# Optimization experiments

Hardware: AMD Instinct MI355X
Metric: run time of the kernel (lower is better)

Reference implementation:

```python
import jax, jax.numpy as jnp
import numpy as np

EPS = 1e-4  # BatchNorm2d eps from source


def binarize(x):
    # brevitas 1-bit quant: sign(x) with sign(0)=+1; straight-through (clipped) estimator
    y = jnp.clip(x, -1.0, 1.0)
    q = jnp.where(x >= 0, 1.0, -1.0).astype(x.dtype)
    return y + jax.lax.stop_gradient(q - y)


def bn(x, g, b, m, v):
    inv = g / jnp.sqrt(v + EPS)
    return x * inv[None, :, None, None] + (b - m * inv)[None, :, None, None]


def conv(x, w, pad):
    return jax.lax.conv_general_dilated(
        x, w, window_strides=(1, 1), padding=[(pad, pad), (pad, pad)],
        dimension_numbers=('NCHW', 'OIHW', 'NCHW'))


def conv_mod(x, w1, bn1, w3, bn3):
    # conv1x1(binary W) -> BN -> binarize act -> conv3x3(binary W) -> BN -> binarize act
    x = conv(x, binarize(w1), 0)
    x = binarize(bn(x, *bn1))
    x = conv(x, binarize(w3), 1)
    x = binarize(bn(x, *bn3))
    return x


def maxpool2(x):
    return jax.lax.reduce_window(x, -jnp.inf, jax.lax.max,
                                 (1, 1, 2, 2), (1, 1, 2, 2), 'VALID')


def setup_inputs() -> dict:
    key = jax.random.key(0)
    ks = jax.random.split(key, 24)
    B, Cin, down, up, H, W = 16, 256, 64, 256, 56, 56
    d = {
        'x':   jax.random.normal(ks[0], (B, Cin, H, W), jnp.float32),
        'w11': jax.random.normal(ks[1], (down, Cin, 1, 1), jnp.float32) * 0.1,
        'w31': jax.random.normal(ks[2], (up, down, 3, 3), jnp.float32) * 0.1,
        'w12': jax.random.normal(ks[3], (down, up, 1, 1), jnp.float32) * 0.1,
        'w32': jax.random.normal(ks[4], (up, down, 3, 3), jnp.float32) * 0.1,
    }
    # BatchNorm params (inference stats): gamma, beta, running mean, running var
    for i, (tag, c) in enumerate([('11', down), ('31', up), ('12', down), ('32', up)]):
        d['g' + tag] = jax.random.uniform(ks[5 + 4 * i], (c,), jnp.float32, 0.5, 1.5)
        d['b' + tag] = jax.random.normal(ks[6 + 4 * i], (c,), jnp.float32) * 0.1
        d['m' + tag] = jax.random.normal(ks[7 + 4 * i], (c,), jnp.float32) * 0.1
        d['v' + tag] = jax.random.uniform(ks[8 + 4 * i], (c,), jnp.float32, 0.5, 1.5)
    return d


def reference(x, w11, w31, w12, w32,
              g11, b11, m11, v11, g31, b31, m31, v31,
              g12, b12, m12, v12, g32, b32, m32, v32):
    h = conv_mod(x, w11, (g11, b11, m11, v11), w31, (g31, b31, m31, v31))
    r = conv_mod(h, w12, (g12, b12, m12, v12), w32, (g32, b32, m32, v32))
    s = binarize(h + r)          # quant_add: re-binarize the residual sum
    return maxpool2(s)           # MaxPool2d(2)
```

## Files before the change

kernel.cpp:

```cpp
#include <hip/hip_runtime.h>
#include <stdint.h>

#pragma clang fp contract(off)


#define HW_   3136
#define NPIX  50176

#define OFF_W31B   0
#define OFF_W12B   18432
#define OFF_W32B   20480
#define OFF_IV11   38912
#define OFF_IV31   39424
#define OFF_IV12   41472
#define OFF_IV32   41984
#define OFF_SGNT   44032
#define OFF_A1     109568
#define OFF_A2     510976
#define OFF_H      912384
#define OFF_S      2518016

__device__ inline float2 mk_ivbt(float g, float b, float m, float v) {
    float inv  = __fdiv_rn(g, __fsqrt_rn(__fadd_rn(v, 1e-4f)));
    float beta = __fsub_rn(b, __fmul_rn(m, inv));
    return make_float2(inv, beta);
}

__global__ __launch_bounds__(256) void k0_all(
    const float* __restrict__ w11, const float* __restrict__ w31,
    const float* __restrict__ w12, const float* __restrict__ w32,
    const float* __restrict__ g11, const float* __restrict__ b11,
    const float* __restrict__ m11, const float* __restrict__ v11,
    const float* __restrict__ g31, const float* __restrict__ b31,
    const float* __restrict__ m31, const float* __restrict__ v31,
    const float* __restrict__ g12, const float* __restrict__ b12,
    const float* __restrict__ m12, const float* __restrict__ v12,
    const float* __restrict__ g32, const float* __restrict__ b32,
    const float* __restrict__ m32, const float* __restrict__ v32,
    uint64_t* __restrict__ W31b, uint64_t* __restrict__ W12b,
    uint64_t* __restrict__ W32b,
    float2* __restrict__ iv11, float2* __restrict__ iv31,
    float2* __restrict__ iv12, float2* __restrict__ iv32,
    float* __restrict__ sgnT)
{
    int blk = blockIdx.x;
    if (blk < 1216) {
        int wid = blk * 4 + (threadIdx.x >> 6);
        int l = threadIdx.x & 63;
        if (wid < 2304) {
            int co = wid / 9, tap = wid % 9;
            uint64_t bits = __ballot(w31[(co * 64 + l) * 9 + tap] >= 0.f);
            if (l == 0) W31b[wid] = bits;
        } else if (wid < 4608) {
            int i = wid - 2304;
            int co = i / 9, tap = i % 9;
            uint64_t bits = __ballot(w32[(co * 64 + l) * 9 + tap] >= 0.f);
            if (l == 0) W32b[i] = bits;
        } else if (wid < 4864) {
            int i = wid - 4608;
            int co = i >> 2, k = i & 3;
            uint64_t bits = __ballot(w12[co * 256 + k * 64 + l] >= 0.f);
            if (l == 0) W12b[i] = bits;
        }
    } else if (blk < 1219) {
        int i = (blk - 1216) * 256 + threadIdx.x;
        if (i < 64)        iv11[i]       = mk_ivbt(g11[i],       b11[i],       m11[i],       v11[i]);
        else if (i < 320)  iv31[i - 64]  = mk_ivbt(g31[i - 64],  b31[i - 64],  m31[i - 64],  v31[i - 64]);
        else if (i < 384)  iv12[i - 320] = mk_ivbt(g12[i - 320], b12[i - 320], m12[i - 320], v12[i - 320]);
        else if (i < 640)  iv32[i - 384] = mk_ivbt(g32[i - 384], b32[i - 384], m32[i - 384], v32[i - 384]);
    } else {
        int t = (blk - 1219) * 256 + threadIdx.x;
        int j = t >> 8, ci = t & 255;
        sgnT[ci * 64 + j] = (w11[t] >= 0.f) ? 1.0f : -1.0f;
    }
}

__global__ __launch_bounds__(512) void k1_conv1(
    const float* __restrict__ x, const float* __restrict__ sgnT,
    const float2* __restrict__ ivbt, unsigned char* __restrict__ A1)
{
    const int l = threadIdx.x & 63;
    const int g = __builtin_amdgcn_readfirstlane(threadIdx.x >> 6);
    const int P = blockIdx.x * 128 + l * 2;
    const int bl = P / HW_;
    const int pxl = P - bl * HW_;
    const float* xp = x + (size_t)bl * (256 * HW_) + pxl;
    const float* sg = sgnT + g * 8;

    float acc[8][2];
#pragma unroll
    for (int j = 0; j < 8; ++j) { acc[j][0] = 0.0f; acc[j][1] = 0.0f; }

    float2 bufA[8], bufB[8];

#define PF(B, CI0)                                                          \
    _Pragma("unroll")                                                       \
    for (int k = 0; k < 8; ++k)                                             \
        B[k] = *(const float2*)(xp + (size_t)((CI0) + k) * HW_);

#define COMP(B, CI0)                                                        \
    _Pragma("unroll")                                                       \
    for (int k = 0; k < 8; ++k) {                                           \
        const float* s_ = sg + ((CI0) + k) * 64;                            \
        _Pragma("unroll")                                                   \
        for (int j = 0; j < 8; ++j) {                                       \
            acc[j][0] = __builtin_fmaf(s_[j], B[k].x, acc[j][0]);           \
            acc[j][1] = __builtin_fmaf(s_[j], B[k].y, acc[j][1]);           \
        }                                                                   \
    }

    for (int cb = 0; cb < 256; cb += 16) {
        __syncthreads();
        if (cb == 0) { PF(bufA, 0) }
        PF(bufB, cb + 8)
        COMP(bufA, cb)
        __syncthreads();
        if (cb + 16 < 256) { PF(bufA, cb + 16) }
        COMP(bufB, cb + 8)
    }
#undef PF
#undef COMP

    unsigned bp0 = 0, bp1 = 0;
#pragma unroll
    for (int j = 0; j < 8; ++j) {
        float2 ib = ivbt[g * 8 + j];
        bp0 |= (__fadd_rn(__fmul_rn(acc[j][0], ib.x), ib.y) >= 0.0f) ? (1u << j) : 0u;
        bp1 |= (__fadd_rn(__fmul_rn(acc[j][1], ib.x), ib.y) >= 0.0f) ? (1u << j) : 0u;
    }
    unsigned char* a = A1 + (size_t)P * 8 + g;
    a[0] = (unsigned char)bp0;
    a[8] = (unsigned char)bp1;
}

template <bool MERGE, bool DO_K3>
__global__ __launch_bounds__(256) void k_conv3b(
    const uint64_t* __restrict__ A, const uint64_t* __restrict__ Wb,
    const float2* __restrict__ ivbt, const uint64_t* __restrict__ Hin,
    uint64_t* __restrict__ Out,
    const uint64_t* __restrict__ W12b, const float2* __restrict__ iv12,
    unsigned short* __restrict__ A2)
{
    __shared__ uint64_t tile[4 * 58];
    __shared__ uint64_t sh4[4][64];
    const int l = threadIdx.x & 63;
    const int wv = threadIdx.x >> 6;
    const int chunk = blockIdx.x;
    const int b = chunk / 49;
    const int hw0 = (chunk % 49) * 64;
    const int r0 = hw0 / 56;
    const int o  = hw0 % 56;
    const int rfirst = r0 - 1;

    {
        int idx = threadIdx.x;
        if (idx < 4 * 58) {
            int rr = idx / 58, cc = idx % 58;
            int gh = rfirst + rr, gw = cc - 1;
            uint64_t v = 0;
            if ((unsigned)gh < 56u && (unsigned)gw < 56u)
                v = A[b * HW_ + gh * 56 + gw];
            tile[idx] = v;
        }
    }

    const int co = wv * 64 + l;
    uint64_t wp[9];
    int c64[9];
#pragma unroll
    for (int t = 0; t < 9; ++t) {
        wp[t] = Wb[co * 9 + t];
        c64[t] = 64 - 2 * (int)__popcll(wp[t]);
    }
    const float2 ib = ivbt[co];

    __syncthreads();

    uint64_t res = 0;
    for (int p = 0; p < 64; ++p) {
        const int inrow2 = (p >= 56 - o) ? 1 : 0;
        const int w = o + p - (inrow2 ? 56 : 0);
        const int row = r0 + inrow2;
        const int rbase = inrow2 * 58;

        int s = 0;
#pragma unroll
        for (int dr = 0; dr < 3; ++dr)
#pragma unroll
            for (int dc = 0; dc < 3; ++dc) {
                uint64_t a = tile[rbase + dr * 58 + w + dc];
                s += (int)__popcll(a ^ wp[dr * 3 + dc]);
            }
        int y = 576 - 2 * s;

        unsigned um = 0;
        if (row == 0)  um |= 0x007u;
        if (row == 55) um |= 0x1C0u;
        if (w == 0)    um |= 0x049u;
        if (w == 55)   um |= 0x124u;
        if (um) {
#pragma unroll
            for (int t = 0; t < 9; ++t)
                if ((um >> t) & 1u) y -= c64[t];
        }

        float val = __fadd_rn(__fmul_rn((float)y, ib.x), ib.y);
        uint64_t word = __ballot(val >= 0.0f);
        res = (l == p) ? word : res;
    }

    size_t oidx = (size_t)wv * NPIX + (size_t)(b * HW_) + hw0 + l;
    if (MERGE) res |= Hin[oidx];
    Out[oidx] = res;

    if (DO_K3) {
        sh4[wv][l] = res;
        __syncthreads();
        uint64_t h0 = sh4[0][l], h1 = sh4[1][l], h2 = sh4[2][l], h3 = sh4[3][l];
        unsigned bits16 = 0;
#pragma unroll
        for (int jj = 0; jj < 16; ++jj) {
            int cq = wv * 16 + jj;
            const uint64_t* wq = W12b + cq * 4;
            int s = (int)(__popcll(h0 ^ wq[0]) + __popcll(h1 ^ wq[1]) +
                          __popcll(h2 ^ wq[2]) + __popcll(h3 ^ wq[3]));
            int y = 256 - 2 * s;
            float2 ibq = iv12[cq];
            float val = __fadd_rn(__fmul_rn((float)y, ibq.x), ibq.y);
            bits16 |= (val >= 0.0f) ? (1u << jj) : 0u;
        }
        A2[(size_t)(b * HW_ + hw0 + l) * 4 + wv] = (unsigned short)bits16;
    }
}

__global__ __launch_bounds__(256) void k4b_pool(
    const uint64_t* __restrict__ S, float* __restrict__ out)
{
    int o = blockIdx.x * 256 + threadIdx.x;
    int ow = o % 28;
    int t = o / 28;
    int oh = t % 28; t /= 28;
    int co = t & 255;
    int b  = t >> 8;
    int k = co >> 6, j = co & 63;
    const uint64_t* Sk = S + (size_t)k * NPIX + (size_t)(b * HW_) + (2 * oh) * 56 + 2 * ow;
    uint64_t s = Sk[0] | Sk[1] | Sk[56] | Sk[57];
    out[o] = ((s >> j) & 1) ? 1.0f : -1.0f;
}

extern "C" void kernel_launch(void* const* d_in, const int* in_sizes, int n_in,
                              void* d_out, int out_size, void* d_ws, size_t ws_size,
                              hipStream_t stream)
{
    const float* x   = (const float*)d_in[0];
    const float* w11 = (const float*)d_in[1];
    const float* w31 = (const float*)d_in[2];
    const float* w12 = (const float*)d_in[3];
    const float* w32 = (const float*)d_in[4];
    const float* g11 = (const float*)d_in[5];
    const float* b11 = (const float*)d_in[6];
    const float* m11 = (const float*)d_in[7];
    const float* v11 = (const float*)d_in[8];
    const float* g31 = (const float*)d_in[9];
    const float* b31 = (const float*)d_in[10];
    const float* m31 = (const float*)d_in[11];
    const float* v31 = (const float*)d_in[12];
    const float* g12 = (const float*)d_in[13];
    const float* b12 = (const float*)d_in[14];
    const float* m12 = (const float*)d_in[15];
    const float* v12 = (const float*)d_in[16];
    const float* g32 = (const float*)d_in[17];
    const float* b32 = (const float*)d_in[18];
    const float* m32 = (const float*)d_in[19];
    const float* v32 = (const float*)d_in[20];

    char* ws = (char*)d_ws;
    uint64_t* W31b = (uint64_t*)(ws + OFF_W31B);
    uint64_t* W12b = (uint64_t*)(ws + OFF_W12B);
    uint64_t* W32b = (uint64_t*)(ws + OFF_W32B);
    float2* iv11 = (float2*)(ws + OFF_IV11);
    float2* iv31 = (float2*)(ws + OFF_IV31);
    float2* iv12 = (float2*)(ws + OFF_IV12);
    float2* iv32 = (float2*)(ws + OFF_IV32);
    float*  sgnT = (float*)(ws + OFF_SGNT);
    uint64_t* A1 = (uint64_t*)(ws + OFF_A1);
    uint64_t* A2 = (uint64_t*)(ws + OFF_A2);
    uint64_t* Hb = (uint64_t*)(ws + OFF_H);
    uint64_t* Sb = (uint64_t*)(ws + OFF_S);

    k0_all<<<dim3(1283), dim3(256), 0, stream>>>(
        w11, w31, w12, w32,
        g11, b11, m11, v11, g31, b31, m31, v31,
        g12, b12, m12, v12, g32, b32, m32, v32,
        W31b, W12b, W32b, iv11, iv31, iv12, iv32, sgnT);

    k1_conv1<<<dim3(392), dim3(512), 0, stream>>>(x, sgnT, iv11, (unsigned char*)A1);

    k_conv3b<false, true><<<dim3(784), dim3(256), 0, stream>>>(
        A1, W31b, iv31, (const uint64_t*)nullptr, Hb,
        W12b, iv12, (unsigned short*)A2);

    k_conv3b<true, false><<<dim3(784), dim3(256), 0, stream>>>(
        A2, W32b, iv32, Hb, Sb,
        (const uint64_t*)nullptr, (const float2*)nullptr, (unsigned short*)nullptr);

    k4b_pool<<<dim3(12544), dim3(256), 0, stream>>>(Sb, (float*)d_out);
}
```

Measured before the change: 119.8 us.

## Restructure conv1x1 so each thread computes all 64 output channels for one pixel

The 1x1 binary-weight conv kernel moves from 512-thread blocks, where 8 waves each computed 8 output channels for two pixels, to single-wave blocks where each thread accumulates all 64 output channels for one pixel. Each input element is now loaded once instead of once per channel group, the block barriers go away, and the 64 sign bits are packed into one uint64 store. The cost is 64 accumulator registers per thread, lower occupancy and only 784 single-wave blocks, which may hide global load latency less well.

```diff
diff --git a/kernel.cpp b/kernel.cpp
--- a/kernel.cpp
+++ b/kernel.cpp
@@ -75,62 +75,54 @@
     }
 }
 
-__global__ __launch_bounds__(512) void k1_conv1(
+__global__ __launch_bounds__(64) void k1_conv1(
     const float* __restrict__ x, const float* __restrict__ sgnT,
-    const float2* __restrict__ ivbt, unsigned char* __restrict__ A1)
-{
-    const int l = threadIdx.x & 63;
-    const int g = __builtin_amdgcn_readfirstlane(threadIdx.x >> 6);
-    const int P = blockIdx.x * 128 + l * 2;
-    const int bl = P / HW_;
-    const int pxl = P - bl * HW_;
-    const float* xp = x + (size_t)bl * (256 * HW_) + pxl;
-    const float* sg = sgnT + g * 8;
-
-    float acc[8][2];
-#pragma unroll
-    for (int j = 0; j < 8; ++j) { acc[j][0] = 0.0f; acc[j][1] = 0.0f; }
-
-    float2 bufA[8], bufB[8];
+    const float2* __restrict__ ivbt, uint64_t* __restrict__ A1)
+{
+    const int l = threadIdx.x;
+    const int blk = blockIdx.x;
+    const int b = blk / 49;
+    const int hw0 = (blk % 49) * 64;
+    const float* xp = x + (size_t)b * 256 * HW_ + hw0 + l;
+
+    float acc[64];
+#pragma unroll
+    for (int j = 0; j < 64; ++j) acc[j] = 0.0f;
+
+    float bufA[8], bufB[8];
 
 #define PF(B, CI0)                                                          \
     _Pragma("unroll")                                                       \
     for (int k = 0; k < 8; ++k)                                             \
-        B[k] = *(const float2*)(xp + (size_t)((CI0) + k) * HW_);
+        B[k] = xp[(size_t)((CI0) + k) * HW_];
 
 #define COMP(B, CI0)                                                        \
     _Pragma("unroll")                                                       \
     for (int k = 0; k < 8; ++k) {                                           \
-        const float* s_ = sg + ((CI0) + k) * 64;                            \
+        const float* s_ = sgnT + ((CI0) + k) * 64;                          \
         _Pragma("unroll")                                                   \
-        for (int j = 0; j < 8; ++j) {                                       \
-            acc[j][0] = __builtin_fmaf(s_[j], B[k].x, acc[j][0]);           \
-            acc[j][1] = __builtin_fmaf(s_[j], B[k].y, acc[j][1]);           \
-        }                                                                   \
-    }
-
+        for (int j = 0; j < 64; ++j)                                        \
+            acc[j] = __builtin_fmaf(s_[j], B[k], acc[j]);                   \
+    }
+
+    PF(bufA, 0)
     for (int cb = 0; cb < 256; cb += 16) {
-        __syncthreads();
-        if (cb == 0) { PF(bufA, 0) }
         PF(bufB, cb + 8)
         COMP(bufA, cb)
-        __syncthreads();
         if (cb + 16 < 256) { PF(bufA, cb + 16) }
         COMP(bufB, cb + 8)
     }
 #undef PF
 #undef COMP
 
-    unsigned bp0 = 0, bp1 = 0;
-#pragma unroll
-    for (int j = 0; j < 8; ++j) {
-        float2 ib = ivbt[g * 8 + j];
-        bp0 |= (__fadd_rn(__fmul_rn(acc[j][0], ib.x), ib.y) >= 0.0f) ? (1u << j) : 0u;
-        bp1 |= (__fadd_rn(__fmul_rn(acc[j][1], ib.x), ib.y) >= 0.0f) ? (1u << j) : 0u;
-    }
-    unsigned char* a = A1 + (size_t)P * 8 + g;
-    a[0] = (unsigned char)bp0;
-    a[8] = (unsigned char)bp1;
+    uint64_t bits = 0;
+#pragma unroll
+    for (int j = 0; j < 64; ++j) {
+        float2 ib = ivbt[j];
+        float val = __fadd_rn(__fmul_rn(acc[j], ib.x), ib.y);
+        bits |= (uint64_t)(val >= 0.0f) << j;
+    }
+    A1[(size_t)blk * 64 + l] = bits;
 }
 
 template <bool MERGE, bool DO_K3>
@@ -294,7 +286,7 @@
         g12, b12, m12, v12, g32, b32, m32, v32,
         W31b, W12b, W32b, iv11, iv31, iv12, iv32, sgnT);
 
-    k1_conv1<<<dim3(392), dim3(512), 0, stream>>>(x, sgnT, iv11, (unsigned char*)A1);
+    k1_conv1<<<dim3(784), dim3(64), 0, stream>>>(x, sgnT, iv11, A1);
 
     k_conv3b<false, true><<<dim3(784), dim3(256), 0, stream>>>(
         A1, W31b, iv31, (const uint64_t*)nullptr, Hb,
```

After: 309.4 us. 2.58x slower.
